# Optimization experiments

Measured on AMD Instinct MI355X. Metric: run time of the kernel, lower is better.

The kernel has to match this reference:

```python
import jax, jax.numpy as jnp
import numpy as np


@jax.custom_vjp
def binarize(w):
    # Deterministic binarization: sign with ties (w==0) mapped to +1,
    # matching tf.where(w >= 0, 1.0, -1.0).
    return jnp.where(w >= 0, 1.0, -1.0).astype(w.dtype)


def _binarize_fwd(w):
    return binarize(w), w


def _binarize_bwd(w, g):
    # Straight-through estimator: pass grad where |w| < 1, else 0.
    return (jnp.where(jnp.abs(w) < 1.0, g, jnp.zeros_like(g)),)


binarize.defvjp(_binarize_fwd, _binarize_bwd)


def setup_inputs() -> dict:
    key = jax.random.key(0)
    kx, kw = jax.random.split(key)
    # NHWC activations
    x = jax.random.normal(kx, (32, 112, 112, 128), dtype=jnp.float32)
    # HWIO kernel (glorot-scale init so values straddle the +/- decision boundary)
    kernel = jax.random.normal(kw, (3, 3, 128, 256), dtype=jnp.float32) * 0.05
    return {"x": x, "kernel": kernel}


def reference(x, kernel):
    wb = binarize(kernel)  # [3,3,Cin,Cout] in {-1,+1}
    return jax.lax.conv_general_dilated(
        x, wb,
        window_strides=(1, 1),
        padding="SAME",
        dimension_numbers=("NHWC", "HWIO", "NHWC"),
    )
```

## Files before the change

kernel.cpp:

```cpp
#include <hip/hip_runtime.h>

typedef __attribute__((ext_vector_type(8))) short short8;
typedef __attribute__((ext_vector_type(4))) float f32x4;
typedef __attribute__((ext_vector_type(4))) unsigned short u16x4;
typedef __attribute__((ext_vector_type(8))) unsigned short u16x8;

#define H 112
#define W 112
#define HP 114
#define WP 114
#define CIN 128
#define COUT 256
#define NPIX (H * W)
#define NIMG 32
#define MTOT (NIMG * NPIX)
#define PADELEMS ((long)NIMG * HP * WP * CIN)
#define NKT 18

__device__ __forceinline__ unsigned short f2bf(float f) {
    unsigned int u = __builtin_bit_cast(unsigned int, f);
    u += 0x7FFFu + ((u >> 16) & 1u);
    return (unsigned short)(u >> 16);
}

__device__ __forceinline__ void gl2lds16(const void* g, void* l) {
    __builtin_amdgcn_global_load_lds(
        (const __attribute__((address_space(1))) unsigned int*)g,
        (__attribute__((address_space(3))) unsigned int*)l,
        16, 0, 0);
}

__global__ void binw2_kernel(const float* __restrict__ kw, unsigned short* __restrict__ bw) {
    int tid = blockIdx.x * 256 + threadIdx.x;
    int c    = tid & 63;
    int cout = (tid >> 6) & 255;
    int kh   = (tid >> 14) & 1;
    int tap  = tid >> 15;
    int cin  = kh * 64 + c;
    float w = kw[(tap * 128 + cin) * 256 + cout];
    bw[tid] = (w >= 0.0f) ? (unsigned short)0x3F80u : (unsigned short)0xBF80u;
}

__global__ void pad_kernel(const float* __restrict__ x, unsigned short* __restrict__ xp) {
    long tid = (long)blockIdx.x * 256 + threadIdx.x;
    if (tid >= PADELEMS / 8) return;
    int c8 = (int)(tid & 15);
    long rem = tid >> 4;
    int wp = (int)(rem % WP); rem /= WP;
    int hp = (int)(rem % HP);
    int n  = (int)(rem / HP);
    u16x8 v = {0, 0, 0, 0, 0, 0, 0, 0};
    if (hp >= 1 && hp <= H && wp >= 1 && wp <= W) {
        const float* s = x + (((long)(n * H + hp - 1) * W + (wp - 1)) * CIN + c8 * 8);
        f32x4 a = *(const f32x4*)s;
        f32x4 b = *(const f32x4*)(s + 4);
        v = (u16x8){ f2bf(a.x), f2bf(a.y), f2bf(a.z), f2bf(a.w),
                     f2bf(b.x), f2bf(b.y), f2bf(b.z), f2bf(b.w) };
    }
    *(u16x8*)(xp + tid * 8) = v;
}

__global__ __launch_bounds__(512, 2)
void conv4_kernel(const unsigned short* __restrict__ xp, const unsigned short* __restrict__ bw,
                  float* __restrict__ out) {
    __shared__ unsigned short As[2][256 * 64];
    __shared__ unsigned short Bs[2][256 * 64];

    const int tid = threadIdx.x;
    const int bm = (blockIdx.x & 7) * 196 + (blockIdx.x >> 3);
    const int lane = tid & 63;
    const int wv = tid >> 6;
    const int wr = wv >> 2;
    const int wc = wv & 3;

    const int r0 = tid >> 3;
    const int c8 = (tid & 7) ^ (r0 & 7);
    long apix[4];
#pragma unroll
    for (int j = 0; j < 4; ++j) {
        int row = r0 + j * 64;
        int p = bm * 256 + row;
        int n = p / NPIX;
        int rem = p - n * NPIX;
        int oh = rem / W, ow = rem - oh * W;
        apix[j] = (long)((n * HP + oh + 1) * WP + (ow + 1)) * CIN;
    }

#define STAGE_HALF(T1, BUF, J) do {                                             \
        const int _tap = (T1) >> 1, _kh = (T1) & 1;                             \
        const long _sh = (long)((_tap / 3 - 1) * WP + (_tap % 3 - 1)) * CIN     \
                         + _kh * 64 + c8 * 8;                                   \
        gl2lds16(xp + apix[J] + _sh, &As[BUF][((J) * 512 + wv * 64) * 8]);      \
        gl2lds16(bw + ((_tap * 2 + _kh) << 14) + r0 * 64 + c8 * 8 + (J) * 4096, \
                 &Bs[BUF][((J) * 512 + wv * 64) * 8]);                          \
    } while (0)

    const int l15 = lane & 15;
    const int lq16 = (lane >> 4) * 16;
    const int arow0 = wr * 128 + l15;
    const int aswz = (arow0 & 7) << 4;
    const int abase = arow0 * 128 + lq16;
    const int brow0 = wc * 64 + l15;
    const int bswz = (brow0 & 7) << 4;
    const int bbase = brow0 * 128 + lq16;

    f32x4 acc[8][4];
#pragma unroll
    for (int m = 0; m < 8; ++m)
#pragma unroll
        for (int n = 0; n < 4; ++n)
            acc[m][n] = (f32x4){0.f, 0.f, 0.f, 0.f};

    STAGE_HALF(0, 0, 0);
    STAGE_HALF(0, 0, 1);
    STAGE_HALF(0, 0, 2);
    STAGE_HALF(0, 0, 3);

    for (int t = 0; t < NKT - 1; ++t) {
        const int cur = t & 1;
        const int nxt = cur ^ 1;
        const char* ab = (const char*)&As[cur][0];
        const char* bb = (const char*)&Bs[cur][0];
        short8 bfrag[4][2];
#pragma unroll
        for (int p = 0; p < 4; ++p) {
            short8 afr[2][2];
            if (p == 0) {
                STAGE_HALF(t + 1, nxt, 0);
                asm volatile("s_waitcnt vmcnt(2)" ::: "memory");
                __builtin_amdgcn_s_barrier();
#pragma unroll
                for (int n = 0; n < 4; ++n)
#pragma unroll
                    for (int kk = 0; kk < 2; ++kk)
                        bfrag[n][kk] = *(const short8*)(bb + ((bbase + n * 2048 + kk * 64) ^ bswz));
#pragma unroll
                for (int mi = 0; mi < 2; ++mi)
#pragma unroll
                    for (int kk = 0; kk < 2; ++kk)
                        afr[mi][kk] = *(const short8*)(ab + ((abase + mi * 2048 + kk * 64) ^ aswz));
            } else {
#pragma unroll
                for (int mi = 0; mi < 2; ++mi)
#pragma unroll
                    for (int kk = 0; kk < 2; ++kk)
                        afr[mi][kk] = *(const short8*)(ab + ((abase + (2 * p + mi) * 2048 + kk * 64) ^ aswz));
                STAGE_HALF(t + 1, nxt, p);
                __builtin_amdgcn_s_barrier();
            }
            asm volatile("s_waitcnt lgkmcnt(0)" ::: "memory");
            __builtin_amdgcn_sched_barrier(0);
            __builtin_amdgcn_s_setprio(1);
#pragma unroll
            for (int mi = 0; mi < 2; ++mi)
#pragma unroll
                for (int n = 0; n < 4; ++n)
#pragma unroll
                    for (int kk = 0; kk < 2; ++kk)
                        acc[2 * p + mi][n] = __builtin_amdgcn_mfma_f32_16x16x32_bf16(
                            afr[mi][kk], bfrag[n][kk], acc[2 * p + mi][n], 0, 0, 0);
            __builtin_amdgcn_s_setprio(0);
            __builtin_amdgcn_s_barrier();
        }
    }

    {
        const int cur = (NKT - 1) & 1;
        const char* ab = (const char*)&As[cur][0];
        const char* bb = (const char*)&Bs[cur][0];
        asm volatile("s_waitcnt vmcnt(0)" ::: "memory");
        __builtin_amdgcn_s_barrier();
        short8 bfrag[4][2];
#pragma unroll
        for (int n = 0; n < 4; ++n)
#pragma unroll
            for (int kk = 0; kk < 2; ++kk)
                bfrag[n][kk] = *(const short8*)(bb + ((bbase + n * 2048 + kk * 64) ^ bswz));
#pragma unroll
        for (int p = 0; p < 4; ++p) {
            short8 afr[2][2];
#pragma unroll
            for (int mi = 0; mi < 2; ++mi)
#pragma unroll
                for (int kk = 0; kk < 2; ++kk)
                    afr[mi][kk] = *(const short8*)(ab + ((abase + (2 * p + mi) * 2048 + kk * 64) ^ aswz));
#pragma unroll
            for (int mi = 0; mi < 2; ++mi)
#pragma unroll
                for (int n = 0; n < 4; ++n)
#pragma unroll
                    for (int kk = 0; kk < 2; ++kk)
                        acc[2 * p + mi][n] = __builtin_amdgcn_mfma_f32_16x16x32_bf16(
                            afr[mi][kk], bfrag[n][kk], acc[2 * p + mi][n], 0, 0, 0);
        }
    }
#undef STAGE_HALF

    const long row0 = (long)bm * 256 + wr * 128 + (lane >> 4) * 4;
    const int col = wc * 64 + (lane & 15);
#pragma unroll
    for (int m = 0; m < 8; ++m)
#pragma unroll
        for (int n = 0; n < 4; ++n)
#pragma unroll
            for (int j = 0; j < 4; ++j)
                out[(row0 + m * 16 + j) * COUT + col + n * 16] = acc[m][n][j];
}

__global__ void binw_kernel(const float* __restrict__ kw, unsigned short* __restrict__ bw) {
    int tid = blockIdx.x * 256 + threadIdx.x;
    int cin5 = tid & 31;
    int cout = (tid >> 5) & 255;
    int kc4  = (tid >> 13) & 3;
    int tap  = tid >> 15;
    int cin  = kc4 * 32 + cin5;
    float w = kw[(tap * 128 + cin) * 256 + cout];
    bw[tid] = (w >= 0.0f) ? (unsigned short)0x3F80u : (unsigned short)0xBF80u;
}

__global__ __launch_bounds__(256, 2)
void conv_fallback_kernel(const float* __restrict__ x, const unsigned short* __restrict__ bw,
                          float* __restrict__ out) {
    __shared__ unsigned short As[128][40];
    __shared__ unsigned short Bs[128][40];
    const int tid = threadIdx.x;
    const int bm = blockIdx.x, bn = blockIdx.y;
    const int lane = tid & 63;
    const int wv = tid >> 6;
    const int wr = wv >> 1, wc = wv & 1;
    const int c4 = (tid & 7) * 4;
    const int rseg = tid >> 3;
    int ohs[4], ows[4], bases[4];
#pragma unroll
    for (int i = 0; i < 4; ++i) {
        int p = bm * 128 + rseg + i * 32;
        int n = p / NPIX;
        int rem = p - n * NPIX;
        int oh = rem / W, ow = rem - oh * W;
        ohs[i] = oh; ows[i] = ow;
        bases[i] = ((n * H + oh) * W + ow) * CIN;
    }
    f32x4 acc[4][4];
#pragma unroll
    for (int m = 0; m < 4; ++m)
#pragma unroll
        for (int n = 0; n < 4; ++n)
            acc[m][n] = (f32x4){0.f, 0.f, 0.f, 0.f};
    const int arow = wr * 64 + (lane & 15);
    const int brow = wc * 64 + (lane & 15);
    const int koff = (lane >> 4) * 8;
    for (int tap = 0; tap < 9; ++tap) {
        const int dh = tap / 3 - 1, dw = tap % 3 - 1;
        const int shift = (dh * W + dw) * CIN;
#pragma unroll
        for (int kc = 0; kc < 4; ++kc) {
            __syncthreads();
#pragma unroll
            for (int i = 0; i < 4; ++i) {
                int ih = ohs[i] + dh, iw = ows[i] + dw;
                bool valid = ((unsigned)ih < (unsigned)H) & ((unsigned)iw < (unsigned)W);
                f32x4 v = {0.f, 0.f, 0.f, 0.f};
                if (valid) v = *(const f32x4*)(x + bases[i] + shift + kc * 32 + c4);
                u16x4 s = { f2bf(v.x), f2bf(v.y), f2bf(v.z), f2bf(v.w) };
                *(u16x4*)&As[rseg + i * 32][c4] = s;
            }
            const unsigned short* bp = bw + tap * 32768 + kc * 8192 + bn * 4096;
#pragma unroll
            for (int j = 0; j < 2; ++j) {
                int idx = tid + j * 256;
                *(u16x8*)&Bs[idx >> 2][(idx & 3) * 8] = *(const u16x8*)(bp + (idx >> 2) * 32 + (idx & 3) * 8);
            }
            __syncthreads();
            short8 af[4], bfr[4];
#pragma unroll
            for (int m = 0; m < 4; ++m)
                af[m] = *(const short8*)&As[arow + m * 16][koff];
#pragma unroll
            for (int n = 0; n < 4; ++n)
                bfr[n] = *(const short8*)&Bs[brow + n * 16][koff];
#pragma unroll
            for (int m = 0; m < 4; ++m)
#pragma unroll
                for (int n = 0; n < 4; ++n)
                    acc[m][n] = __builtin_amdgcn_mfma_f32_16x16x32_bf16(af[m], bfr[n], acc[m][n], 0, 0, 0);
        }
    }
    const long row0 = (long)bm * 128 + wr * 64 + ((lane >> 4) * 4);
    const int col = bn * 128 + wc * 64 + (lane & 15);
#pragma unroll
    for (int m = 0; m < 4; ++m)
#pragma unroll
        for (int n = 0; n < 4; ++n)
#pragma unroll
            for (int j = 0; j < 4; ++j)
                out[(row0 + m * 16 + j) * COUT + col + n * 16] = acc[m][n][j];
}

extern "C" void kernel_launch(void* const* d_in, const int* in_sizes, int n_in,
                              void* d_out, int out_size, void* d_ws, size_t ws_size,
                              hipStream_t stream) {
    const float* x  = (const float*)d_in[0];
    const float* kw = (const float*)d_in[1];
    float* out = (float*)d_out;
    unsigned short* bw = (unsigned short*)d_ws;
    const size_t BW_BYTES = 9 * 2 * 256 * 64 * 2;
    const size_t PAD_BYTES = (size_t)PADELEMS * 2;

    if (ws_size >= BW_BYTES + PAD_BYTES) {
        binw2_kernel<<<(9 * 2 * 256 * 64) / 256, 256, 0, stream>>>(kw, bw);
        unsigned short* xp = (unsigned short*)((char*)d_ws + BW_BYTES);
        pad_kernel<<<(int)((PADELEMS / 8 + 255) / 256), 256, 0, stream>>>(x, xp);
        conv4_kernel<<<MTOT / 256, 512, 0, stream>>>(xp, bw, out);
    } else {
        binw_kernel<<<(9 * 256 * 128) / 256, 256, 0, stream>>>(kw, bw);
        dim3 grid(MTOT / 128, COUT / 128);
        conv_fallback_kernel<<<grid, 256, 0, stream>>>(x, bw, out);
    }
}
```

Before: 360.1 us.

## Shrink conv block tile to 128x128 with 256 threads and split Cout across blocks

Replaces the 256x256-tile, 512-thread implicit-GEMM conv kernel with a 128x128-tile, 256-thread kernel. Each block now covers half of Cout, and the grid is twice as wide with a swizzled block index. Staging is regrouped into two halves per K step. The aim is smaller LDS use and more blocks for occupancy and load balance, at the cost of less data reuse per block and loading each activation tile twice.

```diff
diff --git a/kernel.cpp b/kernel.cpp
--- a/kernel.cpp
+++ b/kernel.cpp
@@ -60,61 +60,63 @@
     *(u16x8*)(xp + tid * 8) = v;
 }
 
-__global__ __launch_bounds__(512, 2)
-void conv4_kernel(const unsigned short* __restrict__ xp, const unsigned short* __restrict__ bw,
+__global__ __launch_bounds__(256, 2)
+void conv5_kernel(const unsigned short* __restrict__ xp, const unsigned short* __restrict__ bw,
                   float* __restrict__ out) {
-    __shared__ unsigned short As[2][256 * 64];
-    __shared__ unsigned short Bs[2][256 * 64];
+    __shared__ unsigned short As[2][128 * 64];
+    __shared__ unsigned short Bs[2][128 * 64];
 
     const int tid = threadIdx.x;
-    const int bm = (blockIdx.x & 7) * 196 + (blockIdx.x >> 3);
+    const int swz = (blockIdx.x & 7) * 784 + (blockIdx.x >> 3);
+    const int bm = swz >> 1;
+    const int bn = swz & 1;
     const int lane = tid & 63;
     const int wv = tid >> 6;
-    const int wr = wv >> 2;
-    const int wc = wv & 3;
+    const int wr = wv >> 1, wc = wv & 1;
 
     const int r0 = tid >> 3;
     const int c8 = (tid & 7) ^ (r0 & 7);
     long apix[4];
 #pragma unroll
     for (int j = 0; j < 4; ++j) {
-        int row = r0 + j * 64;
-        int p = bm * 256 + row;
+        int row = r0 + j * 32;
+        int p = bm * 128 + row;
         int n = p / NPIX;
         int rem = p - n * NPIX;
         int oh = rem / W, ow = rem - oh * W;
         apix[j] = (long)((n * HP + oh + 1) * WP + (ow + 1)) * CIN;
     }
 
-#define STAGE_HALF(T1, BUF, J) do {                                             \
+#define STAGE_J(T1, BUF, J) do {                                                \
         const int _tap = (T1) >> 1, _kh = (T1) & 1;                             \
         const long _sh = (long)((_tap / 3 - 1) * WP + (_tap % 3 - 1)) * CIN     \
                          + _kh * 64 + c8 * 8;                                   \
-        gl2lds16(xp + apix[J] + _sh, &As[BUF][((J) * 512 + wv * 64) * 8]);      \
-        gl2lds16(bw + ((_tap * 2 + _kh) << 14) + r0 * 64 + c8 * 8 + (J) * 4096, \
-                 &Bs[BUF][((J) * 512 + wv * 64) * 8]);                          \
+        gl2lds16(xp + apix[J] + _sh, &As[BUF][((J) * 256 + wv * 64) * 8]);      \
+        gl2lds16(bw + ((_tap * 2 + _kh) << 14) + bn * 8192                      \
+                    + (r0 + (J) * 32) * 64 + c8 * 8,                            \
+                 &Bs[BUF][((J) * 256 + wv * 64) * 8]);                          \
     } while (0)
 
     const int l15 = lane & 15;
     const int lq16 = (lane >> 4) * 16;
-    const int arow0 = wr * 128 + l15;
+    const int arow0 = wr * 64 + l15;
     const int aswz = (arow0 & 7) << 4;
     const int abase = arow0 * 128 + lq16;
     const int brow0 = wc * 64 + l15;
     const int bswz = (brow0 & 7) << 4;
     const int bbase = brow0 * 128 + lq16;
 
-    f32x4 acc[8][4];
-#pragma unroll
-    for (int m = 0; m < 8; ++m)
+    f32x4 acc[4][4];
+#pragma unroll
+    for (int m = 0; m < 4; ++m)
 #pragma unroll
         for (int n = 0; n < 4; ++n)
             acc[m][n] = (f32x4){0.f, 0.f, 0.f, 0.f};
 
-    STAGE_HALF(0, 0, 0);
-    STAGE_HALF(0, 0, 1);
-    STAGE_HALF(0, 0, 2);
-    STAGE_HALF(0, 0, 3);
+    STAGE_J(0, 0, 0);
+    STAGE_J(0, 0, 1);
+    STAGE_J(0, 0, 2);
+    STAGE_J(0, 0, 3);
 
     for (int t = 0; t < NKT - 1; ++t) {
         const int cur = t & 1;
@@ -122,32 +124,23 @@
         const char* ab = (const char*)&As[cur][0];
         const char* bb = (const char*)&Bs[cur][0];
         short8 bfrag[4][2];
-#pragma unroll
-        for (int p = 0; p < 4; ++p) {
+
+        STAGE_J(t + 1, nxt, 0);
+        STAGE_J(t + 1, nxt, 1);
+        asm volatile("s_waitcnt vmcnt(4)" ::: "memory");
+        __builtin_amdgcn_s_barrier();
+#pragma unroll
+        for (int n = 0; n < 4; ++n)
+#pragma unroll
+            for (int kk = 0; kk < 2; ++kk)
+                bfrag[n][kk] = *(const short8*)(bb + ((bbase + n * 2048 + kk * 64) ^ bswz));
+        {
             short8 afr[2][2];
-            if (p == 0) {
-                STAGE_HALF(t + 1, nxt, 0);
-                asm volatile("s_waitcnt vmcnt(2)" ::: "memory");
-                __builtin_amdgcn_s_barrier();
-#pragma unroll
-                for (int n = 0; n < 4; ++n)
-#pragma unroll
-                    for (int kk = 0; kk < 2; ++kk)
-                        bfrag[n][kk] = *(const short8*)(bb + ((bbase + n * 2048 + kk * 64) ^ bswz));
-#pragma unroll
-                for (int mi = 0; mi < 2; ++mi)
-#pragma unroll
-                    for (int kk = 0; kk < 2; ++kk)
-                        afr[mi][kk] = *(const short8*)(ab + ((abase + mi * 2048 + kk * 64) ^ aswz));
-            } else {
-#pragma unroll
-                for (int mi = 0; mi < 2; ++mi)
-#pragma unroll
-                    for (int kk = 0; kk < 2; ++kk)
-                        afr[mi][kk] = *(const short8*)(ab + ((abase + (2 * p + mi) * 2048 + kk * 64) ^ aswz));
-                STAGE_HALF(t + 1, nxt, p);
-                __builtin_amdgcn_s_barrier();
-            }
+#pragma unroll
+            for (int mi = 0; mi < 2; ++mi)
+#pragma unroll
+                for (int kk = 0; kk < 2; ++kk)
+                    afr[mi][kk] = *(const short8*)(ab + ((abase + mi * 2048 + kk * 64) ^ aswz));
             asm volatile("s_waitcnt lgkmcnt(0)" ::: "memory");
             __builtin_amdgcn_sched_barrier(0);
             __builtin_amdgcn_s_setprio(1);
@@ -157,8 +150,33 @@
                 for (int n = 0; n < 4; ++n)
 #pragma unroll
                     for (int kk = 0; kk < 2; ++kk)
-                        acc[2 * p + mi][n] = __builtin_amdgcn_mfma_f32_16x16x32_bf16(
-                            afr[mi][kk], bfrag[n][kk], acc[2 * p + mi][n], 0, 0, 0);
+                        acc[mi][n] = __builtin_amdgcn_mfma_f32_16x16x32_bf16(
+                            afr[mi][kk], bfrag[n][kk], acc[mi][n], 0, 0, 0);
+            __builtin_amdgcn_s_setprio(0);
+            __builtin_amdgcn_s_barrier();
+        }
+
+        {
+            short8 afr[2][2];
+#pragma unroll
+            for (int mi = 0; mi < 2; ++mi)
+#pragma unroll
+                for (int kk = 0; kk < 2; ++kk)
+                    afr[mi][kk] = *(const short8*)(ab + ((abase + (2 + mi) * 2048 + kk * 64) ^ aswz));
+            STAGE_J(t + 1, nxt, 2);
+            STAGE_J(t + 1, nxt, 3);
+            __builtin_amdgcn_s_barrier();
+            asm volatile("s_waitcnt lgkmcnt(0)" ::: "memory");
+            __builtin_amdgcn_sched_barrier(0);
+            __builtin_amdgcn_s_setprio(1);
+#pragma unroll
+            for (int mi = 0; mi < 2; ++mi)
+#pragma unroll
+                for (int n = 0; n < 4; ++n)
+#pragma unroll
+                    for (int kk = 0; kk < 2; ++kk)
+                        acc[2 + mi][n] = __builtin_amdgcn_mfma_f32_16x16x32_bf16(
+                            afr[mi][kk], bfrag[n][kk], acc[2 + mi][n], 0, 0, 0);
             __builtin_amdgcn_s_setprio(0);
             __builtin_amdgcn_s_barrier();
         }
@@ -177,29 +195,25 @@
             for (int kk = 0; kk < 2; ++kk)
                 bfrag[n][kk] = *(const short8*)(bb + ((bbase + n * 2048 + kk * 64) ^ bswz));
 #pragma unroll
-        for (int p = 0; p < 4; ++p) {
-            short8 afr[2][2];
-#pragma unroll
-            for (int mi = 0; mi < 2; ++mi)
+        for (int m = 0; m < 4; ++m) {
+            short8 afr[2];
+#pragma unroll
+            for (int kk = 0; kk < 2; ++kk)
+                afr[kk] = *(const short8*)(ab + ((abase + m * 2048 + kk * 64) ^ aswz));
+#pragma unroll
+            for (int n = 0; n < 4; ++n)
 #pragma unroll
                 for (int kk = 0; kk < 2; ++kk)
-                    afr[mi][kk] = *(const short8*)(ab + ((abase + (2 * p + mi) * 2048 + kk * 64) ^ aswz));
-#pragma unroll
-            for (int mi = 0; mi < 2; ++mi)
-#pragma unroll
-                for (int n = 0; n < 4; ++n)
-#pragma unroll
-                    for (int kk = 0; kk < 2; ++kk)
-                        acc[2 * p + mi][n] = __builtin_amdgcn_mfma_f32_16x16x32_bf16(
-                            afr[mi][kk], bfrag[n][kk], acc[2 * p + mi][n], 0, 0, 0);
+                    acc[m][n] = __builtin_amdgcn_mfma_f32_16x16x32_bf16(
+                        afr[kk], bfrag[n][kk], acc[m][n], 0, 0, 0);
         }
     }
-#undef STAGE_HALF
-
-    const long row0 = (long)bm * 256 + wr * 128 + (lane >> 4) * 4;
-    const int col = wc * 64 + (lane & 15);
-#pragma unroll
-    for (int m = 0; m < 8; ++m)
+#undef STAGE_J
+
+    const long row0 = (long)bm * 128 + wr * 64 + (lane >> 4) * 4;
+    const int col = bn * 128 + wc * 64 + l15;
+#pragma unroll
+    for (int m = 0; m < 4; ++m)
 #pragma unroll
         for (int n = 0; n < 4; ++n)
 #pragma unroll
@@ -310,7 +324,7 @@
         binw2_kernel<<<(9 * 2 * 256 * 64) / 256, 256, 0, stream>>>(kw, bw);
         unsigned short* xp = (unsigned short*)((char*)d_ws + BW_BYTES);
         pad_kernel<<<(int)((PADELEMS / 8 + 255) / 256), 256, 0, stream>>>(x, xp);
-        conv4_kernel<<<MTOT / 256, 512, 0, stream>>>(xp, bw, out);
+        conv5_kernel<<<(MTOT / 128) * 2, 256, 0, stream>>>(xp, bw, out);
     } else {
         binw_kernel<<<(9 * 256 * 128) / 256, 256, 0, stream>>>(kw, bw);
         dim3 grid(MTOT / 128, COUT / 128);
```

Result: faster. 342.6 us (-4.9%).

## Make conv kernel persistent with cross-tile prefetch of the next M tile

Applied to the files above, without the earlier changes.

Replaces the one-block-per-tile launch with a fixed grid of 256 persistent blocks, each walking 6 or 7 consecutive 256-row output tiles. The last K step of each tile prefetches the first K chunk of the next tile, so global loads overlap the previous tile's compute and the store of its accumulators. This removes the per-tile prologue and epilogue bubbles and the tail effect of 1568 small blocks. The cost is load imbalance between blocks with 6 and 7 tiles, and the original L2-friendly interleaved block ordering is dropped.

```diff
diff --git a/kernel.cpp b/kernel.cpp
--- a/kernel.cpp
+++ b/kernel.cpp
@@ -16,6 +16,7 @@
 #define MTOT (NIMG * NPIX)
 #define PADELEMS ((long)NIMG * HP * WP * CIN)
 #define NKT 18
+#define NTILES (MTOT / 256)
 
 __device__ __forceinline__ unsigned short f2bf(float f) {
     unsigned int u = __builtin_bit_cast(unsigned int, f);
@@ -61,13 +62,16 @@
 }
 
 __global__ __launch_bounds__(512, 2)
-void conv4_kernel(const unsigned short* __restrict__ xp, const unsigned short* __restrict__ bw,
+void conv6_kernel(const unsigned short* __restrict__ xp, const unsigned short* __restrict__ bw,
                   float* __restrict__ out) {
     __shared__ unsigned short As[2][256 * 64];
     __shared__ unsigned short Bs[2][256 * 64];
 
     const int tid = threadIdx.x;
-    const int bm = (blockIdx.x & 7) * 196 + (blockIdx.x >> 3);
+    const int bid = blockIdx.x;
+    const int tStart = bid * 6 + (bid < 32 ? bid : 32);
+    const int tCnt = 6 + (bid < 32 ? 1 : 0);
+
     const int lane = tid & 63;
     const int wv = tid >> 6;
     const int wr = wv >> 2;
@@ -75,22 +79,25 @@
 
     const int r0 = tid >> 3;
     const int c8 = (tid & 7) ^ (r0 & 7);
-    long apix[4];
-#pragma unroll
-    for (int j = 0; j < 4; ++j) {
-        int row = r0 + j * 64;
-        int p = bm * 256 + row;
-        int n = p / NPIX;
-        int rem = p - n * NPIX;
-        int oh = rem / W, ow = rem - oh * W;
-        apix[j] = (long)((n * HP + oh + 1) * WP + (ow + 1)) * CIN;
-    }
-
-#define STAGE_HALF(T1, BUF, J) do {                                             \
-        const int _tap = (T1) >> 1, _kh = (T1) & 1;                             \
+
+    long apix[4], napix[4];
+#define CALC_APIX(DST, BM) do {                                                 \
+        _Pragma("unroll")                                                       \
+        for (int j = 0; j < 4; ++j) {                                           \
+            int row = r0 + j * 64;                                              \
+            int p = (BM) * 256 + row;                                           \
+            int n = p / NPIX;                                                   \
+            int rem = p - n * NPIX;                                             \
+            int oh = rem / W, ow = rem - oh * W;                                \
+            DST[j] = (long)((n * HP + oh + 1) * WP + (ow + 1)) * CIN;           \
+        }                                                                       \
+    } while (0)
+
+#define STAGE_J(KT, BUF, J, AP) do {                                            \
+        const int _tap = (KT) >> 1, _kh = (KT) & 1;                             \
         const long _sh = (long)((_tap / 3 - 1) * WP + (_tap % 3 - 1)) * CIN     \
                          + _kh * 64 + c8 * 8;                                   \
-        gl2lds16(xp + apix[J] + _sh, &As[BUF][((J) * 512 + wv * 64) * 8]);      \
+        gl2lds16(xp + AP[J] + _sh, &As[BUF][((J) * 512 + wv * 64) * 8]);        \
         gl2lds16(bw + ((_tap * 2 + _kh) << 14) + r0 * 64 + c8 * 8 + (J) * 4096, \
                  &Bs[BUF][((J) * 512 + wv * 64) * 8]);                          \
     } while (0)
@@ -111,100 +118,107 @@
         for (int n = 0; n < 4; ++n)
             acc[m][n] = (f32x4){0.f, 0.f, 0.f, 0.f};
 
-    STAGE_HALF(0, 0, 0);
-    STAGE_HALF(0, 0, 1);
-    STAGE_HALF(0, 0, 2);
-    STAGE_HALF(0, 0, 3);
-
-    for (int t = 0; t < NKT - 1; ++t) {
-        const int cur = t & 1;
-        const int nxt = cur ^ 1;
-        const char* ab = (const char*)&As[cur][0];
-        const char* bb = (const char*)&Bs[cur][0];
-        short8 bfrag[4][2];
-#pragma unroll
-        for (int p = 0; p < 4; ++p) {
-            short8 afr[2][2];
-            if (p == 0) {
-                STAGE_HALF(t + 1, nxt, 0);
+    CALC_APIX(apix, tStart);
+    STAGE_J(0, 0, 0, apix);
+    STAGE_J(0, 0, 1, apix);
+    STAGE_J(0, 0, 2, apix);
+    STAGE_J(0, 0, 3, apix);
+
+    for (int tile = 0; tile < tCnt; ++tile) {
+        const int bm = tStart + tile;
+        const bool moreTiles = (tile + 1 < tCnt);
+        if (moreTiles) CALC_APIX(napix, bm + 1);
+
+        for (int kt = 0; kt < NKT; ++kt) {
+            const int cur = kt & 1;
+            const int nxt = cur ^ 1;
+            const int ktn = (kt == NKT - 1) ? 0 : kt + 1;
+            const long* ap = (kt == NKT - 1) ? napix : apix;
+            const bool hn = (kt < NKT - 1) || moreTiles;
+            const char* ab = (const char*)&As[cur][0];
+            const char* bb = (const char*)&Bs[cur][0];
+            short8 bfrag[4][2];
+
+            if (hn) {
+                STAGE_J(ktn, nxt, 0, ap);
                 asm volatile("s_waitcnt vmcnt(2)" ::: "memory");
-                __builtin_amdgcn_s_barrier();
-#pragma unroll
-                for (int n = 0; n < 4; ++n)
-#pragma unroll
-                    for (int kk = 0; kk < 2; ++kk)
-                        bfrag[n][kk] = *(const short8*)(bb + ((bbase + n * 2048 + kk * 64) ^ bswz));
+            } else {
+                asm volatile("s_waitcnt vmcnt(0)" ::: "memory");
+            }
+            __builtin_amdgcn_s_barrier();
+#pragma unroll
+            for (int n = 0; n < 4; ++n)
+#pragma unroll
+                for (int kk = 0; kk < 2; ++kk)
+                    bfrag[n][kk] = *(const short8*)(bb + ((bbase + n * 2048 + kk * 64) ^ bswz));
+            {
+                short8 afr[2][2];
 #pragma unroll
                 for (int mi = 0; mi < 2; ++mi)
 #pragma unroll
                     for (int kk = 0; kk < 2; ++kk)
                         afr[mi][kk] = *(const short8*)(ab + ((abase + mi * 2048 + kk * 64) ^ aswz));
-            } else {
+                asm volatile("s_waitcnt lgkmcnt(0)" ::: "memory");
+                __builtin_amdgcn_sched_barrier(0);
+                __builtin_amdgcn_s_setprio(1);
+#pragma unroll
+                for (int mi = 0; mi < 2; ++mi)
+#pragma unroll
+                    for (int n = 0; n < 4; ++n)
+#pragma unroll
+                        for (int kk = 0; kk < 2; ++kk)
+                            acc[mi][n] = __builtin_amdgcn_mfma_f32_16x16x32_bf16(
+                                afr[mi][kk], bfrag[n][kk], acc[mi][n], 0, 0, 0);
+                __builtin_amdgcn_s_setprio(0);
+                __builtin_amdgcn_s_barrier();
+            }
+
+#pragma unroll
+            for (int p = 1; p < 4; ++p) {
+                short8 afr[2][2];
 #pragma unroll
                 for (int mi = 0; mi < 2; ++mi)
 #pragma unroll
                     for (int kk = 0; kk < 2; ++kk)
                         afr[mi][kk] = *(const short8*)(ab + ((abase + (2 * p + mi) * 2048 + kk * 64) ^ aswz));
-                STAGE_HALF(t + 1, nxt, p);
+                if (hn) STAGE_J(ktn, nxt, p, ap);
                 __builtin_amdgcn_s_barrier();
-            }
-            asm volatile("s_waitcnt lgkmcnt(0)" ::: "memory");
-            __builtin_amdgcn_sched_barrier(0);
-            __builtin_amdgcn_s_setprio(1);
-#pragma unroll
-            for (int mi = 0; mi < 2; ++mi)
-#pragma unroll
-                for (int n = 0; n < 4; ++n)
-#pragma unroll
-                    for (int kk = 0; kk < 2; ++kk)
-                        acc[2 * p + mi][n] = __builtin_amdgcn_mfma_f32_16x16x32_bf16(
-                            afr[mi][kk], bfrag[n][kk], acc[2 * p + mi][n], 0, 0, 0);
-            __builtin_amdgcn_s_setprio(0);
-            __builtin_amdgcn_s_barrier();
+                asm volatile("s_waitcnt lgkmcnt(0)" ::: "memory");
+                __builtin_amdgcn_sched_barrier(0);
+                __builtin_amdgcn_s_setprio(1);
+#pragma unroll
+                for (int mi = 0; mi < 2; ++mi)
+#pragma unroll
+                    for (int n = 0; n < 4; ++n)
+#pragma unroll
+                        for (int kk = 0; kk < 2; ++kk)
+                            acc[2 * p + mi][n] = __builtin_amdgcn_mfma_f32_16x16x32_bf16(
+                                afr[mi][kk], bfrag[n][kk], acc[2 * p + mi][n], 0, 0, 0);
+                __builtin_amdgcn_s_setprio(0);
+                __builtin_amdgcn_s_barrier();
+            }
         }
-    }
-
-    {
-        const int cur = (NKT - 1) & 1;
-        const char* ab = (const char*)&As[cur][0];
-        const char* bb = (const char*)&Bs[cur][0];
-        asm volatile("s_waitcnt vmcnt(0)" ::: "memory");
-        __builtin_amdgcn_s_barrier();
-        short8 bfrag[4][2];
-#pragma unroll
-        for (int n = 0; n < 4; ++n)
-#pragma unroll
-            for (int kk = 0; kk < 2; ++kk)
-                bfrag[n][kk] = *(const short8*)(bb + ((bbase + n * 2048 + kk * 64) ^ bswz));
-#pragma unroll
-        for (int p = 0; p < 4; ++p) {
-            short8 afr[2][2];
-#pragma unroll
-            for (int mi = 0; mi < 2; ++mi)
-#pragma unroll
-                for (int kk = 0; kk < 2; ++kk)
-                    afr[mi][kk] = *(const short8*)(ab + ((abase + (2 * p + mi) * 2048 + kk * 64) ^ aswz));
-#pragma unroll
-            for (int mi = 0; mi < 2; ++mi)
-#pragma unroll
-                for (int n = 0; n < 4; ++n)
-#pragma unroll
-                    for (int kk = 0; kk < 2; ++kk)
-                        acc[2 * p + mi][n] = __builtin_amdgcn_mfma_f32_16x16x32_bf16(
-                            afr[mi][kk], bfrag[n][kk], acc[2 * p + mi][n], 0, 0, 0);
-        }
-    }
-#undef STAGE_HALF
-
-    const long row0 = (long)bm * 256 + wr * 128 + (lane >> 4) * 4;
-    const int col = wc * 64 + (lane & 15);
-#pragma unroll
-    for (int m = 0; m < 8; ++m)
-#pragma unroll
-        for (int n = 0; n < 4; ++n)
-#pragma unroll
-            for (int j = 0; j < 4; ++j)
-                out[(row0 + m * 16 + j) * COUT + col + n * 16] = acc[m][n][j];
+
+        const long row0 = (long)bm * 256 + wr * 128 + (lane >> 4) * 4;
+        const int col = wc * 64 + l15;
+#pragma unroll
+        for (int m = 0; m < 8; ++m)
+#pragma unroll
+            for (int n = 0; n < 4; ++n)
+#pragma unroll
+                for (int j = 0; j < 4; ++j)
+                    out[(row0 + m * 16 + j) * COUT + col + n * 16] = acc[m][n][j];
+#pragma unroll
+        for (int m = 0; m < 8; ++m)
+#pragma unroll
+            for (int n = 0; n < 4; ++n)
+                acc[m][n] = (f32x4){0.f, 0.f, 0.f, 0.f};
+#pragma unroll
+        for (int j = 0; j < 4; ++j)
+            apix[j] = napix[j];
+    }
+#undef STAGE_J
+#undef CALC_APIX
 }
 
 __global__ void binw_kernel(const float* __restrict__ kw, unsigned short* __restrict__ bw) {
@@ -310,7 +324,7 @@
         binw2_kernel<<<(9 * 2 * 256 * 64) / 256, 256, 0, stream>>>(kw, bw);
         unsigned short* xp = (unsigned short*)((char*)d_ws + BW_BYTES);
         pad_kernel<<<(int)((PADELEMS / 8 + 255) / 256), 256, 0, stream>>>(x, xp);
-        conv4_kernel<<<MTOT / 256, 512, 0, stream>>>(xp, bw, out);
+        conv6_kernel<<<256, 512, 0, stream>>>(xp, bw, out);
     } else {
         binw_kernel<<<(9 * 256 * 128) / 256, 256, 0, stream>>>(kw, bw);
         dim3 grid(MTOT / 128, COUT / 128);
```

Result: no change. 365.7 us (+1.6%).
